# Optimization experiments

Hardware: AMD Instinct MI355X
Metric: run time of the kernel (lower is better)

The kernel has to match this reference:

```python
import jax, jax.numpy as jnp
import numpy as np

L, D, H, B, S, V = 4, 1024, 16, 8, 512, 32000
DK = D // H          # per-head dim = 64; only head 0 is ever used (bug in source)
FF = 4 * D
EPS = 1e-3           # keras BatchNormalization default epsilon


def _bn(x, gamma, beta, mean, var):
    # inference-mode BatchNorm over last axis (keras default)
    return gamma * (x - mean) * jax.lax.rsqrt(var + EPS) + beta


def setup_inputs() -> dict:
    key = jax.random.key(0)
    keys = iter(jax.random.split(key, 40))

    def rn(shape, scale=0.02):
        return jax.random.normal(next(keys), shape, jnp.float32) * scale

    sequence = jax.random.randint(next(keys), (B, S), 0, V, dtype=jnp.int32)

    # standard sinusoidal positional encoding table [S, D]
    pos = np.arange(S)[:, None].astype(np.float32)
    i = np.arange(D)[None, :]
    angle = pos / np.power(10000.0, (2 * (i // 2)) / D).astype(np.float32)
    pes = np.where(i % 2 == 0, np.sin(angle), np.cos(angle)).astype(np.float32)

    return {
        "sequence": sequence,
        "emb": rn((V, D)),
        "pes": jnp.asarray(pes),
        # single-head attention params (head 0 only, per the source bug), stacked over layers
        "wq": rn((L, D, DK)), "bq": jnp.zeros((L, DK)),
        "wk": rn((L, D, DK)), "bk": jnp.zeros((L, DK)),
        "wv": rn((L, D, DK)), "bv": jnp.zeros((L, DK)),
        "wo": rn((L, DK, D)), "bo": jnp.zeros((L, D)),
        "att_gamma": 1.0 + rn((L, D), 0.1), "att_beta": rn((L, D), 0.1),
        "att_mean": rn((L, D), 0.1), "att_var": jnp.ones((L, D)),
        "w1": rn((L, D, FF)), "bff1": jnp.zeros((L, FF)),
        "w2": rn((L, FF, D)), "bff2": jnp.zeros((L, D)),
        "ffn_gamma": 1.0 + rn((L, D), 0.1), "ffn_beta": rn((L, D), 0.1),
        "ffn_mean": rn((L, D), 0.1), "ffn_var": jnp.ones((L, D)),
    }


def reference(sequence, emb, pes, wq, bq, wk, bk, wv, bv, wo, bo,
              att_gamma, att_beta, att_mean, att_var,
              w1, bff1, w2, bff2,
              ffn_gamma, ffn_beta, ffn_mean, ffn_var):
    # embedding + positional bug: only pes[i, 0] (a scalar per position) is added
    x = emb[sequence] + pes[:S, 0:1][None]          # [B, S, D]
    scale = 1.0 / jnp.sqrt(jnp.float32(DK))
    for l in range(L):
        q = x @ wq[l] + bq[l]                       # [B, S, DK]
        k = x @ wk[l] + bk[l]
        v = x @ wv[l] + bv[l]
        score = jnp.einsum('bqd,bkd->bqk', q, k) * scale
        head = jax.nn.softmax(score, axis=-1) @ v   # [B, S, DK]
        att = head @ wo[l] + bo[l]                  # [B, S, D]
        x = _bn(x + att, att_gamma[l], att_beta[l], att_mean[l], att_var[l])
        ffn = jax.nn.relu(x @ w1[l] + bff1[l]) @ w2[l] + bff2[l]
        x = _bn(x + ffn, ffn_gamma[l], ffn_beta[l], ffn_mean[l], ffn_var[l])
    return x
```

## Files before the change

kernel.cpp:

```cpp
#include <hip/hip_runtime.h>
#include <hip/hip_bf16.h>
#include <stdint.h>

#define L_  4
#define D_  1024
#define DK_ 64
#define B_  8
#define S_  512
#define FF_ 4096
#define M_  (B_*S_)
#define EPS_ 1e-3f
#define QKVN_ 256

typedef __bf16 bf16_t;
typedef bf16_t bf16x8 __attribute__((ext_vector_type(8)));
typedef float  f32x4  __attribute__((ext_vector_type(4)));

__device__ __forceinline__ bf16_t f2b(float f) {
    union { float f; uint32_t u; } v; v.f = f;
    uint32_t r = v.u + 0x7fff + ((v.u >> 16) & 1);
    uint16_t h = (uint16_t)(r >> 16);
    bf16_t o; __builtin_memcpy(&o, &h, 2); return o;
}

__device__ __forceinline__ void gl2lds16(const bf16_t* g, bf16_t* l) {
    __builtin_amdgcn_global_load_lds(
        (__attribute__((address_space(1))) void*)g,
        (__attribute__((address_space(3))) void*)l, 16, 0, 0);
}

__global__ void embed_kernel(const int* __restrict__ seq, const float* __restrict__ emb,
                             const float* __restrict__ pes, float* __restrict__ x,
                             bf16_t* __restrict__ xb) {
    int idx = blockIdx.x * 256 + threadIdx.x;
    int md  = idx >> 10;
    int d   = idx & (D_ - 1);
    int s   = md & (S_ - 1);
    float v = emb[(size_t)seq[md] * D_ + d] + pes[s * D_];
    x[idx] = v;
    xb[idx] = f2b(v);
}

__device__ __forceinline__ void tile_tr(const float* __restrict__ src, bf16_t* __restrict__ dst,
                                        int K, int N, int kb, int nb, float (*t)[33]) {
    int k0 = kb * 32, n0 = nb * 32;
    int c = threadIdx.x & 31, r = threadIdx.x >> 5;
    #pragma unroll
    for (int i = 0; i < 4; i++)
        t[r + i * 8][c] = src[(size_t)(k0 + r + i * 8) * N + n0 + c];
    __syncthreads();
    #pragma unroll
    for (int i = 0; i < 4; i++)
        dst[(size_t)(n0 + r + i * 8) * K + k0 + c] = f2b(t[c][r + i * 8]);
}

__global__ void prep_weights(const float* __restrict__ wq, const float* __restrict__ wk,
                             const float* __restrict__ wv, const float* __restrict__ wo,
                             const float* __restrict__ w1, const float* __restrict__ w2,
                             const float* __restrict__ bq, const float* __restrict__ bk,
                             const float* __restrict__ bv,
                             bf16_t* __restrict__ wqkvt, bf16_t* __restrict__ wot,
                             bf16_t* __restrict__ w1t, bf16_t* __restrict__ w2t,
                             float* __restrict__ bqkv) {
    __shared__ float t[32][33];
    int bid = blockIdx.x;
    if (bid < 4096) {
        tile_tr(w1, w1t, D_, FF_, bid & 31, bid >> 5, t);
    } else if (bid < 8192) {
        int rem = bid - 4096;
        tile_tr(w2, w2t, FF_, D_, rem & 127, rem >> 7, t);
    } else if (bid < 8384) {
        int rem = bid - 8192;
        int which = rem >> 6; rem &= 63;
        const float* src = which == 0 ? wq : (which == 1 ? wk : wv);
        tile_tr(src, wqkvt + (size_t)which * 64 * D_, D_, DK_, rem & 31, rem >> 5, t);
    } else if (bid < 8448) {
        int rem = bid - 8384;
        tile_tr(wo, wot, DK_, D_, rem & 1, rem >> 1, t);
    } else if (bid < 8464) {
        int rem = bid - 8448;
        bf16_t* z = wqkvt + (size_t)192 * D_ + rem * 4096;
        for (int i = threadIdx.x; i < 4096; i += 256) z[i] = (bf16_t)0.f;
    } else {
        int n = threadIdx.x;
        float v = 0.f;
        if      (n <  64) v = bq[n];
        else if (n < 128) v = bk[n - 64];
        else if (n < 192) v = bv[n - 128];
        bqkv[n] = v;
    }
}

template<int MODE>
__global__ __launch_bounds__(256)
void gemm_mfma3(const bf16_t* __restrict__ A, const bf16_t* __restrict__ Bt,
                const float* __restrict__ bias, bf16_t* __restrict__ Cb,
                const float* __restrict__ Xin, float* __restrict__ Xf, bf16_t* __restrict__ Xb,
                const float* __restrict__ g, const float* __restrict__ bb,
                const float* __restrict__ mu, const float* __restrict__ var,
                int N, int K, int kChunk, size_t strideZ) {
    __shared__ bf16_t As[128 * 64];
    __shared__ bf16_t Bs[128 * 64];
    const int tid  = threadIdx.x;
    const int w    = tid >> 6, lane = tid & 63;
    const int wm   = w >> 1,   wn   = w & 1;
    const int lm   = lane & 15, quad = lane >> 4;
    const int m0 = blockIdx.y * 128, n0 = blockIdx.x * 128;
    const int kBeg = blockIdx.z * kChunk, kEnd = kBeg + kChunk;
    const int lrow = lane >> 3;
    const int lk   = (lane & 7) ^ lrow;

    f32x4 acc[4][4];
    #pragma unroll
    for (int i = 0; i < 4; i++)
        #pragma unroll
        for (int j = 0; j < 4; j++) acc[i][j] = (f32x4){0.f, 0.f, 0.f, 0.f};

    for (int k0 = kBeg; k0 < kEnd; k0 += 64) {
        #pragma unroll
        for (int i = 0; i < 4; i++) {
            const int r0 = w * 32 + i * 8;
            gl2lds16(A  + (size_t)(m0 + r0 + lrow) * K + k0 + lk * 8, As + r0 * 64);
            gl2lds16(Bt + (size_t)(n0 + r0 + lrow) * K + k0 + lk * 8, Bs + r0 * 64);
        }
        __syncthreads();
        #pragma unroll
        for (int s = 0; s < 2; s++) {
            bf16x8 af[4], bfr[4];
            #pragma unroll
            for (int mi = 0; mi < 4; mi++) {
                const int ra = wm * 64 + mi * 16 + lm;
                af[mi] = *(const bf16x8*)(As + ra * 64 + (((s * 4 + quad) ^ (lm & 7)) * 8));
            }
            #pragma unroll
            for (int ni = 0; ni < 4; ni++) {
                const int rb = wn * 64 + ni * 16 + lm;
                bfr[ni] = *(const bf16x8*)(Bs + rb * 64 + (((s * 4 + quad) ^ (lm & 7)) * 8));
            }
            #pragma unroll
            for (int mi = 0; mi < 4; mi++)
                #pragma unroll
                for (int ni = 0; ni < 4; ni++)
                    acc[mi][ni] = __builtin_amdgcn_mfma_f32_16x16x32_bf16(
                        af[mi], bfr[ni], acc[mi][ni], 0, 0, 0);
        }
        __syncthreads();
    }

    bf16_t* Pz = (MODE == 2) ? Cb + (size_t)blockIdx.z * strideZ : Cb;

    #pragma unroll
    for (int ni = 0; ni < 4; ni++) {
        const int col = n0 + wn * 64 + ni * 16 + lm;
        float bv = 0.f, gv = 0.f, bbv = 0.f, muv = 0.f, rsv = 0.f;
        if (MODE != 2) bv = bias[col];
        if (MODE == 3) {
            gv = g[col]; bbv = bb[col]; muv = mu[col];
            rsv = rsqrtf(var[col] + EPS_);
        }
        #pragma unroll
        for (int mi = 0; mi < 4; mi++) {
            const int rbase = m0 + wm * 64 + mi * 16 + quad * 4;
            #pragma unroll
            for (int r = 0; r < 4; r++) {
                const size_t idx = (size_t)(rbase + r) * N + col;
                float v = acc[mi][ni][r] + bv;
                if (MODE == 1) Cb[idx] = f2b(fmaxf(v, 0.f));
                if (MODE == 2) Pz[idx] = f2b(v);
                if (MODE == 3) {
                    float s = Xin[idx] + v;
                    float o = gv * (s - muv) * rsv + bbv;
                    Xf[idx] = o;
                    Xb[idx] = f2b(o);
                }
            }
        }
    }
}

__global__ void qkv_reduce(const bf16_t* __restrict__ P, const float* __restrict__ bias,
                           bf16_t* __restrict__ dst) {
    int idx = blockIdx.x * 256 + threadIdx.x;
    int n = idx & (QKVN_ - 1);
    float s = bias[n];
    #pragma unroll
    for (int zz = 0; zz < 4; zz++) s += (float)P[(size_t)zz * M_ * QKVN_ + idx];
    dst[idx] = f2b(s);
}

__global__ void vt_kernel(const bf16_t* __restrict__ qkv, bf16_t* __restrict__ Vt) {
    int b = blockIdx.y, k0 = blockIdx.x * 64;
    const bf16_t* vb = qkv + (size_t)b * S_ * QKVN_ + 128;
    __shared__ bf16_t t[64][65];
    int c = threadIdx.x & 63, r4 = threadIdx.x >> 6;
    #pragma unroll
    for (int i = 0; i < 16; i++) {
        int k = i * 4 + r4;
        t[c][k] = vb[(size_t)(k0 + k) * QKVN_ + c];
    }
    __syncthreads();
    #pragma unroll
    for (int i = 0; i < 16; i++) {
        int d = i * 4 + r4;
        Vt[((size_t)b * DK_ + d) * S_ + k0 + c] = t[d][c];
    }
}

__global__ __launch_bounds__(256)
void attn_fused(const bf16_t* __restrict__ qkv, const bf16_t* __restrict__ Vt,
                bf16_t* __restrict__ hdb) {
    const int b  = blockIdx.y;
    const int i0 = blockIdx.x * 64;
    const bf16_t* qb  = qkv + (size_t)b * S_ * QKVN_;
    const bf16_t* kb  = qb + 64;
    const bf16_t* vtb = Vt + (size_t)b * DK_ * S_;

    __shared__ bf16_t Ps[8 * 64 * 64];
    __shared__ bf16_t Vs[8 * 64 * 64];
    __shared__ float  rowred[4][64];

    const int tid  = threadIdx.x;
    const int w    = tid >> 6, lane = tid & 63;
    const int lm   = lane & 15, quad = lane >> 4;
    const int lrow = lane >> 3;
    const int lk   = (lane & 7) ^ lrow;

    #pragma unroll
    for (int i = 0; i < 16; i++) {
        const int r0 = w * 16 + (i & 1) * 8;
        const int kt = i >> 1;
        gl2lds16(vtb + (size_t)(r0 + lrow) * S_ + kt * 64 + lk * 8,
                 Vs + kt * 4096 + r0 * 64);
    }

    f32x4 acc[4][8];
    #pragma unroll
    for (int mi = 0; mi < 4; mi++)
        #pragma unroll
        for (int ni = 0; ni < 8; ni++) acc[mi][ni] = (f32x4){0.f, 0.f, 0.f, 0.f};

    #pragma unroll
    for (int s = 0; s < 2; s++) {
        bf16x8 af[4], bfr[8];
        #pragma unroll
        for (int mi = 0; mi < 4; mi++)
            af[mi] = *(const bf16x8*)(qb + (size_t)(i0 + mi * 16 + lm) * QKVN_ + s * 32 + quad * 8);
        #pragma unroll
        for (int ni = 0; ni < 8; ni++)
            bfr[ni] = *(const bf16x8*)(kb + (size_t)(w * 128 + ni * 16 + lm) * QKVN_ + s * 32 + quad * 8);
        #pragma unroll
        for (int mi = 0; mi < 4; mi++)
            #pragma unroll
            for (int ni = 0; ni < 8; ni++)
                acc[mi][ni] = __builtin_amdgcn_mfma_f32_16x16x32_bf16(
                    af[mi], bfr[ni], acc[mi][ni], 0, 0, 0);
    }
    #pragma unroll
    for (int mi = 0; mi < 4; mi++)
        #pragma unroll
        for (int ni = 0; ni < 8; ni++) acc[mi][ni] *= 0.125f;

    float rmax[4][4];
    #pragma unroll
    for (int mi = 0; mi < 4; mi++)
        #pragma unroll
        for (int r = 0; r < 4; r++) {
            float m = acc[mi][0][r];
            #pragma unroll
            for (int ni = 1; ni < 8; ni++) m = fmaxf(m, acc[mi][ni][r]);
            #pragma unroll
            for (int off = 1; off < 16; off <<= 1) m = fmaxf(m, __shfl_xor(m, off, 64));
            rmax[mi][r] = m;
        }
    if (lm == 0) {
        #pragma unroll
        for (int mi = 0; mi < 4; mi++)
            #pragma unroll
            for (int r = 0; r < 4; r++)
                rowred[w][mi * 16 + quad * 4 + r] = rmax[mi][r];
    }
    __syncthreads();
    float gmax[4][4];
    #pragma unroll
    for (int mi = 0; mi < 4; mi++)
        #pragma unroll
        for (int r = 0; r < 4; r++) {
            const int row = mi * 16 + quad * 4 + r;
            gmax[mi][r] = fmaxf(fmaxf(rowred[0][row], rowred[1][row]),
                                fmaxf(rowred[2][row], rowred[3][row]));
        }
    __syncthreads();

    float rsum[4][4];
    #pragma unroll
    for (int mi = 0; mi < 4; mi++)
        #pragma unroll
        for (int r = 0; r < 4; r++) rsum[mi][r] = 0.f;
    #pragma unroll
    for (int mi = 0; mi < 4; mi++) {
        #pragma unroll
        for (int ni = 0; ni < 8; ni++) {
            const int key = w * 128 + ni * 16 + lm;
            const int kt  = key >> 6;
            const int ck  = (key >> 3) & 7;
            #pragma unroll
            for (int r = 0; r < 4; r++) {
                const int m = mi * 16 + quad * 4 + r;
                float p = __expf(acc[mi][ni][r] - gmax[mi][r]);
                bf16_t pb = f2b(p);
                rsum[mi][r] += (float)pb;
                Ps[kt * 4096 + m * 64 + ((ck ^ (m & 7)) * 8) + (key & 7)] = pb;
            }
        }
    }
    #pragma unroll
    for (int mi = 0; mi < 4; mi++)
        #pragma unroll
        for (int r = 0; r < 4; r++) {
            float s = rsum[mi][r];
            #pragma unroll
            for (int off = 1; off < 16; off <<= 1) s += __shfl_xor(s, off, 64);
            rsum[mi][r] = s;
        }
    if (lm == 0) {
        #pragma unroll
        for (int mi = 0; mi < 4; mi++)
            #pragma unroll
            for (int r = 0; r < 4; r++)
                rowred[w][mi * 16 + quad * 4 + r] = rsum[mi][r];
    }
    __syncthreads();

    f32x4 accO[4];
    #pragma unroll
    for (int ni = 0; ni < 4; ni++) accO[ni] = (f32x4){0.f, 0.f, 0.f, 0.f};
    #pragma unroll
    for (int ks = 0; ks < 16; ks++) {
        const int kt = ks >> 1;
        const int co = (ks & 1) * 4 + quad;
        bf16x8 af = *(const bf16x8*)(Ps + kt * 4096 + (w * 16 + lm) * 64 + ((co ^ (lm & 7)) * 8));
        #pragma unroll
        for (int ni = 0; ni < 4; ni++) {
            bf16x8 bfr = *(const bf16x8*)(Vs + kt * 4096 + (ni * 16 + lm) * 64 + ((co ^ (lm & 7)) * 8));
            accO[ni] = __builtin_amdgcn_mfma_f32_16x16x32_bf16(af, bfr, accO[ni], 0, 0, 0);
        }
    }

    #pragma unroll
    for (int r = 0; r < 4; r++) {
        const int row = w * 16 + quad * 4 + r;
        const float tot = rowred[0][row] + rowred[1][row] + rowred[2][row] + rowred[3][row];
        const float inv = 1.0f / tot;
        #pragma unroll
        for (int ni = 0; ni < 4; ni++)
            hdb[(size_t)(b * S_ + i0 + row) * DK_ + ni * 16 + lm] = f2b(accO[ni][r] * inv);
    }
}

__global__ void bn_residual2(const float* __restrict__ x, const bf16_t* __restrict__ p,
                             const float* __restrict__ bias,
                             const float* __restrict__ g, const float* __restrict__ b,
                             const float* __restrict__ mu, const float* __restrict__ var,
                             float* __restrict__ dst, bf16_t* __restrict__ dstb) {
    int idx = blockIdx.x * 256 + threadIdx.x;
    int d = idx & (D_ - 1);
    float r = bias[d] + (float)p[idx] + (float)p[(size_t)M_ * D_ + idx];
    float s = x[idx] + r;
    float o = g[d] * (s - mu[d]) * rsqrtf(var[d] + EPS_) + b[d];
    dst[idx] = o;
    dstb[idx] = f2b(o);
}

extern "C" void kernel_launch(void* const* d_in, const int* in_sizes, int n_in,
                              void* d_out, int out_size, void* d_ws, size_t ws_size,
                              hipStream_t stream) {
    const int*   seq = (const int*)  d_in[0];
    const float* emb = (const float*)d_in[1];
    const float* pes = (const float*)d_in[2];
    const float* wq  = (const float*)d_in[3];
    const float* bq  = (const float*)d_in[4];
    const float* wk  = (const float*)d_in[5];
    const float* bk  = (const float*)d_in[6];
    const float* wv  = (const float*)d_in[7];
    const float* bv  = (const float*)d_in[8];
    const float* wo  = (const float*)d_in[9];
    const float* bo  = (const float*)d_in[10];
    const float* ag  = (const float*)d_in[11];
    const float* ab  = (const float*)d_in[12];
    const float* am  = (const float*)d_in[13];
    const float* av  = (const float*)d_in[14];
    const float* w1  = (const float*)d_in[15];
    const float* b1  = (const float*)d_in[16];
    const float* w2  = (const float*)d_in[17];
    const float* b2  = (const float*)d_in[18];
    const float* fg  = (const float*)d_in[19];
    const float* fb  = (const float*)d_in[20];
    const float* fm  = (const float*)d_in[21];
    const float* fv  = (const float*)d_in[22];
    float* out = (float*)d_out;

    char* p = (char*)d_ws;
    auto alloc = [&](size_t bytes) { char* q = p; p += (bytes + 255) & ~(size_t)255; return q; };
    float*  X     = (float*) alloc((size_t)M_ * D_ * 4);
    bf16_t* Xb    = (bf16_t*)alloc((size_t)M_ * D_ * 2);
    bf16_t* qkvb  = (bf16_t*)alloc((size_t)M_ * QKVN_ * 2);
    bf16_t* Vtb   = (bf16_t*)alloc((size_t)B_ * DK_ * S_ * 2);
    bf16_t* hdb   = (bf16_t*)alloc((size_t)M_ * DK_ * 2);
    bf16_t* hb    = (bf16_t*)alloc((size_t)M_ * FF_ * 2);
    bf16_t* w1t   = (bf16_t*)alloc((size_t)FF_ * D_ * 2);
    bf16_t* w2t   = (bf16_t*)alloc((size_t)D_ * FF_ * 2);
    bf16_t* wqkvt = (bf16_t*)alloc((size_t)QKVN_ * D_ * 2);
    bf16_t* wot   = (bf16_t*)alloc((size_t)D_ * DK_ * 2);
    float*  bqkv  = (float*) alloc(QKVN_ * 4);

    embed_kernel<<<M_ * D_ / 256, 256, 0, stream>>>(seq, emb, pes, X, Xb);

    for (int l = 0; l < L_; l++) {
        prep_weights<<<8465, 256, 0, stream>>>(
            wq + (size_t)l * D_ * DK_, wk + (size_t)l * D_ * DK_, wv + (size_t)l * D_ * DK_,
            wo + (size_t)l * DK_ * D_, w1 + (size_t)l * D_ * FF_, w2 + (size_t)l * FF_ * D_,
            bq + l * DK_, bk + l * DK_, bv + l * DK_,
            wqkvt, wot, w1t, w2t, bqkv);

        gemm_mfma3<2><<<dim3(QKVN_ / 128, M_ / 128, 4), 256, 0, stream>>>(
            Xb, wqkvt, nullptr, (bf16_t*)out, nullptr, nullptr, nullptr,
            nullptr, nullptr, nullptr, nullptr, QKVN_, D_, D_ / 4, (size_t)M_ * QKVN_);
        qkv_reduce<<<M_ * QKVN_ / 256, 256, 0, stream>>>((const bf16_t*)out, bqkv, qkvb);

        vt_kernel<<<dim3(S_ / 64, B_), 256, 0, stream>>>(qkvb, Vtb);
        attn_fused<<<dim3(S_ / 64, B_), 256, 0, stream>>>(qkvb, Vtb, hdb);

        gemm_mfma3<3><<<dim3(D_ / 128, M_ / 128, 1), 256, 0, stream>>>(
            hdb, wot, bo + l * D_, nullptr, X, X, Xb,
            ag + l * D_, ab + l * D_, am + l * D_, av + l * D_, D_, DK_, DK_, 0);

        gemm_mfma3<1><<<dim3(FF_ / 128, M_ / 128, 1), 256, 0, stream>>>(
            Xb, w1t, b1 + l * FF_, hb, nullptr, nullptr, nullptr,
            nullptr, nullptr, nullptr, nullptr, FF_, D_, D_, 0);

        gemm_mfma3<2><<<dim3(D_ / 128, M_ / 128, 2), 256, 0, stream>>>(
            hb, w2t, nullptr, (bf16_t*)out, nullptr, nullptr, nullptr,
            nullptr, nullptr, nullptr, nullptr, D_, FF_, FF_ / 2, (size_t)M_ * D_);

        bn_residual2<<<M_ * D_ / 256, 256, 0, stream>>>(
            X, (const bf16_t*)out, b2 + l * D_,
            fg + l * D_, fb + l * D_, fm + l * D_, fv + l * D_, X, Xb);
        if (l == L_ - 1)
            hipMemcpyAsync(out, X, (size_t)M_ * D_ * 4, hipMemcpyDeviceToDevice, stream);
    }
}
```

Measured before the change: 919.3 us.

## Batch weight prep, fuse QKV reduce with V transpose, write final output directly

Weight transposition for all layers now runs in one launch before the layer loop instead of once per layer, so there are fewer launches and the prep work is better batched. The QKV split-K reduce and the V transpose are merged into one kernel that also folds the 1/sqrt(dk) scale into Q, which removes the scaling pass in attention. The FFN partial sums now go to a separate workspace buffer, so the last BatchNorm writes straight to the output and the final device copy and bf16 store are dropped. This needs more workspace for the per-layer weights, and the fused reduce kernel launches far fewer blocks than before.

```diff
diff --git a/kernel.cpp b/kernel.cpp
--- a/kernel.cpp
+++ b/kernel.cpp
@@ -11,6 +11,7 @@
 #define M_  (B_*S_)
 #define EPS_ 1e-3f
 #define QKVN_ 256
+#define PREPB_ 8465
 
 typedef __bf16 bf16_t;
 typedef bf16_t bf16x8 __attribute__((ext_vector_type(8)));
@@ -63,31 +64,44 @@
                              bf16_t* __restrict__ w1t, bf16_t* __restrict__ w2t,
                              float* __restrict__ bqkv) {
     __shared__ float t[32][33];
-    int bid = blockIdx.x;
+    const int l   = blockIdx.x / PREPB_;
+    int bid = blockIdx.x % PREPB_;
+    const float* wq_ = wq + (size_t)l * D_ * DK_;
+    const float* wk_ = wk + (size_t)l * D_ * DK_;
+    const float* wv_ = wv + (size_t)l * D_ * DK_;
+    const float* wo_ = wo + (size_t)l * DK_ * D_;
+    const float* w1_ = w1 + (size_t)l * D_ * FF_;
+    const float* w2_ = w2 + (size_t)l * FF_ * D_;
+    bf16_t* wqkvt_ = wqkvt + (size_t)l * QKVN_ * D_;
+    bf16_t* wot_   = wot   + (size_t)l * D_ * DK_;
+    bf16_t* w1t_   = w1t   + (size_t)l * FF_ * D_;
+    bf16_t* w2t_   = w2t   + (size_t)l * D_ * FF_;
+    float*  bqkv_  = bqkv  + l * QKVN_;
+
     if (bid < 4096) {
-        tile_tr(w1, w1t, D_, FF_, bid & 31, bid >> 5, t);
+        tile_tr(w1_, w1t_, D_, FF_, bid & 31, bid >> 5, t);
     } else if (bid < 8192) {
         int rem = bid - 4096;
-        tile_tr(w2, w2t, FF_, D_, rem & 127, rem >> 7, t);
+        tile_tr(w2_, w2t_, FF_, D_, rem & 127, rem >> 7, t);
     } else if (bid < 8384) {
         int rem = bid - 8192;
         int which = rem >> 6; rem &= 63;
-        const float* src = which == 0 ? wq : (which == 1 ? wk : wv);
-        tile_tr(src, wqkvt + (size_t)which * 64 * D_, D_, DK_, rem & 31, rem >> 5, t);
+        const float* src = which == 0 ? wq_ : (which == 1 ? wk_ : wv_);
+        tile_tr(src, wqkvt_ + (size_t)which * 64 * D_, D_, DK_, rem & 31, rem >> 5, t);
     } else if (bid < 8448) {
         int rem = bid - 8384;
-        tile_tr(wo, wot, DK_, D_, rem & 1, rem >> 1, t);
+        tile_tr(wo_, wot_, DK_, D_, rem & 1, rem >> 1, t);
     } else if (bid < 8464) {
         int rem = bid - 8448;
-        bf16_t* z = wqkvt + (size_t)192 * D_ + rem * 4096;
+        bf16_t* z = wqkvt_ + (size_t)192 * D_ + rem * 4096;
         for (int i = threadIdx.x; i < 4096; i += 256) z[i] = (bf16_t)0.f;
     } else {
         int n = threadIdx.x;
         float v = 0.f;
-        if      (n <  64) v = bq[n];
-        else if (n < 128) v = bk[n - 64];
-        else if (n < 192) v = bv[n - 128];
-        bqkv[n] = v;
+        if      (n <  64) v = bq[l * DK_ + n];
+        else if (n < 128) v = bk[l * DK_ + n - 64];
+        else if (n < 192) v = bv[l * DK_ + n - 128];
+        bqkv_[n] = v;
     }
 }
 
@@ -178,31 +192,49 @@
     }
 }
 
-__global__ void qkv_reduce(const bf16_t* __restrict__ P, const float* __restrict__ bias,
-                           bf16_t* __restrict__ dst) {
-    int idx = blockIdx.x * 256 + threadIdx.x;
-    int n = idx & (QKVN_ - 1);
-    float s = bias[n];
-    #pragma unroll
-    for (int zz = 0; zz < 4; zz++) s += (float)P[(size_t)zz * M_ * QKVN_ + idx];
-    dst[idx] = f2b(s);
-}
-
-__global__ void vt_kernel(const bf16_t* __restrict__ qkv, bf16_t* __restrict__ Vt) {
-    int b = blockIdx.y, k0 = blockIdx.x * 64;
-    const bf16_t* vb = qkv + (size_t)b * S_ * QKVN_ + 128;
-    __shared__ bf16_t t[64][65];
-    int c = threadIdx.x & 63, r4 = threadIdx.x >> 6;
+__global__ void qkv_finish(const bf16_t* __restrict__ P, const float* __restrict__ bias,
+                           bf16_t* __restrict__ qkvb, bf16_t* __restrict__ Vt) {
+    const int b = blockIdx.y, k0 = blockIdx.x * 64;
+    __shared__ bf16_t t[64][66];
+    const int tid = threadIdx.x;
+    const int c8  = tid & 31;
+    const int r0  = tid >> 5;
+    if (c8 < 24) {
+        const int n = c8 * 8;
+        float bv[8];
+        #pragma unroll
+        for (int j = 0; j < 8; j++) bv[j] = bias[n + j];
+        const float qs = (c8 < 8) ? 0.125f : 1.0f;
+        #pragma unroll
+        for (int p = 0; p < 8; p++) {
+            const int r = r0 + p * 8;
+            const size_t m = (size_t)(b * S_ + k0 + r);
+            float s[8];
+            #pragma unroll
+            for (int j = 0; j < 8; j++) s[j] = bv[j];
+            #pragma unroll
+            for (int z = 0; z < 4; z++) {
+                bf16x8 v = *(const bf16x8*)(P + (size_t)z * M_ * QKVN_ + m * QKVN_ + n);
+                #pragma unroll
+                for (int j = 0; j < 8; j++) s[j] += (float)v[j];
+            }
+            bf16x8 o;
+            #pragma unroll
+            for (int j = 0; j < 8; j++) o[j] = f2b(s[j] * qs);
+            if (c8 < 16) {
+                *(bf16x8*)(qkvb + m * QKVN_ + n) = o;
+            } else {
+                #pragma unroll
+                for (int j = 0; j < 8; j++) t[r][(n - 128) + j] = o[j];
+            }
+        }
+    }
+    __syncthreads();
     #pragma unroll
     for (int i = 0; i < 16; i++) {
-        int k = i * 4 + r4;
-        t[c][k] = vb[(size_t)(k0 + k) * QKVN_ + c];
-    }
-    __syncthreads();
-    #pragma unroll
-    for (int i = 0; i < 16; i++) {
-        int d = i * 4 + r4;
-        Vt[((size_t)b * DK_ + d) * S_ + k0 + c] = t[d][c];
+        int idx = tid + i * 256;
+        int d = idx >> 6, c = idx & 63;
+        Vt[((size_t)b * DK_ + d) * S_ + k0 + c] = t[c][d];
     }
 }
 
@@ -255,10 +287,6 @@
                 acc[mi][ni] = __builtin_amdgcn_mfma_f32_16x16x32_bf16(
                     af[mi], bfr[ni], acc[mi][ni], 0, 0, 0);
     }
-    #pragma unroll
-    for (int mi = 0; mi < 4; mi++)
-        #pragma unroll
-        for (int ni = 0; ni < 8; ni++) acc[mi][ni] *= 0.125f;
 
     float rmax[4][4];
     #pragma unroll
@@ -368,7 +396,7 @@
     float s = x[idx] + r;
     float o = g[d] * (s - mu[d]) * rsqrtf(var[d] + EPS_) + b[d];
     dst[idx] = o;
-    dstb[idx] = f2b(o);
+    if (dstb) dstb[idx] = f2b(o);
 }
 
 extern "C" void kernel_launch(void* const* d_in, const int* in_sizes, int n_in,
@@ -407,45 +435,49 @@
     bf16_t* Vtb   = (bf16_t*)alloc((size_t)B_ * DK_ * S_ * 2);
     bf16_t* hdb   = (bf16_t*)alloc((size_t)M_ * DK_ * 2);
     bf16_t* hb    = (bf16_t*)alloc((size_t)M_ * FF_ * 2);
-    bf16_t* w1t   = (bf16_t*)alloc((size_t)FF_ * D_ * 2);
-    bf16_t* w2t   = (bf16_t*)alloc((size_t)D_ * FF_ * 2);
-    bf16_t* wqkvt = (bf16_t*)alloc((size_t)QKVN_ * D_ * 2);
-    bf16_t* wot   = (bf16_t*)alloc((size_t)D_ * DK_ * 2);
-    float*  bqkv  = (float*) alloc(QKVN_ * 4);
+    bf16_t* w1t   = (bf16_t*)alloc((size_t)L_ * FF_ * D_ * 2);
+    bf16_t* w2t   = (bf16_t*)alloc((size_t)L_ * D_ * FF_ * 2);
+    bf16_t* wqkvt = (bf16_t*)alloc((size_t)L_ * QKVN_ * D_ * 2);
+    bf16_t* wot   = (bf16_t*)alloc((size_t)L_ * D_ * DK_ * 2);
+    bf16_t* part  = (bf16_t*)alloc((size_t)2 * M_ * D_ * 2);
+    float*  bqkv  = (float*) alloc((size_t)L_ * QKVN_ * 4);
 
     embed_kernel<<<M_ * D_ / 256, 256, 0, stream>>>(seq, emb, pes, X, Xb);
 
+    prep_weights<<<L_ * PREPB_, 256, 0, stream>>>(
+        wq, wk, wv, wo, w1, w2, bq, bk, bv, wqkvt, wot, w1t, w2t, bqkv);
+
     for (int l = 0; l < L_; l++) {
-        prep_weights<<<8465, 256, 0, stream>>>(
-            wq + (size_t)l * D_ * DK_, wk + (size_t)l * D_ * DK_, wv + (size_t)l * D_ * DK_,
-            wo + (size_t)l * DK_ * D_, w1 + (size_t)l * D_ * FF_, w2 + (size_t)l * FF_ * D_,
-            bq + l * DK_, bk + l * DK_, bv + l * DK_,
-            wqkvt, wot, w1t, w2t, bqkv);
+        const bf16_t* wqkvt_ = wqkvt + (size_t)l * QKVN_ * D_;
+        const bf16_t* wot_   = wot   + (size_t)l * D_ * DK_;
+        const bf16_t* w1t_   = w1t   + (size_t)l * FF_ * D_;
+        const bf16_t* w2t_   = w2t   + (size_t)l * D_ * FF_;
+        const float*  bqkv_  = bqkv  + l * QKVN_;
 
         gemm_mfma3<2><<<dim3(QKVN_ / 128, M_ / 128, 4), 256, 0, stream>>>(
-            Xb, wqkvt, nullptr, (bf16_t*)out, nullptr, nullptr, nullptr,
+            Xb, wqkvt_, nullptr, (bf16_t*)out, nullptr, nullptr, nullptr,
             nullptr, nullptr, nullptr, nullptr, QKVN_, D_, D_ / 4, (size_t)M_ * QKVN_);
-        qkv_reduce<<<M_ * QKVN_ / 256, 256, 0, stream>>>((const bf16_t*)out, bqkv, qkvb);
-
-        vt_kernel<<<dim3(S_ / 64, B_), 256, 0, stream>>>(qkvb, Vtb);
+
+        qkv_finish<<<dim3(S_ / 64, B_), 256, 0, stream>>>(
+            (const bf16_t*)out, bqkv_, qkvb, Vtb);
+
         attn_fused<<<dim3(S_ / 64, B_), 256, 0, stream>>>(qkvb, Vtb, hdb);
 
         gemm_mfma3<3><<<dim3(D_ / 128, M_ / 128, 1), 256, 0, stream>>>(
-            hdb, wot, bo + l * D_, nullptr, X, X, Xb,
+            hdb, wot_, bo + l * D_, nullptr, X, X, Xb,
             ag + l * D_, ab + l * D_, am + l * D_, av + l * D_, D_, DK_, DK_, 0);
 
         gemm_mfma3<1><<<dim3(FF_ / 128, M_ / 128, 1), 256, 0, stream>>>(
-            Xb, w1t, b1 + l * FF_, hb, nullptr, nullptr, nullptr,
+            Xb, w1t_, b1 + l * FF_, hb, nullptr, nullptr, nullptr,
             nullptr, nullptr, nullptr, nullptr, FF_, D_, D_, 0);
 
         gemm_mfma3<2><<<dim3(D_ / 128, M_ / 128, 2), 256, 0, stream>>>(
-            hb, w2t, nullptr, (bf16_t*)out, nullptr, nullptr, nullptr,
+            hb, w2t_, nullptr, part, nullptr, nullptr, nullptr,
             nullptr, nullptr, nullptr, nullptr, D_, FF_, FF_ / 2, (size_t)M_ * D_);
 
         bn_residual2<<<M_ * D_ / 256, 256, 0, stream>>>(
-            X, (const bf16_t*)out, b2 + l * D_,
-            fg + l * D_, fb + l * D_, fm + l * D_, fv + l * D_, X, Xb);
-        if (l == L_ - 1)
-            hipMemcpyAsync(out, X, (size_t)M_ * D_ * 4, hipMemcpyDeviceToDevice, stream);
-    }
-}
+            X, part, b2 + l * D_,
+            fg + l * D_, fb + l * D_, fm + l * D_, fv + l * D_,
+            (l == L_ - 1) ? out : X, (l == L_ - 1) ? nullptr : Xb);
+    }
+}
```

After: 930.5 us. Within noise of the previous version (+1.2%).
